# Optimization experiments

Hardware: AMD Instinct MI355X
Metric: run time of the kernel (lower is better)

Reference implementation:

```python
import jax, jax.numpy as jnp
import numpy as np
from jax import lax
from jax.scipy.special import logsumexp

V, E, H, S, L = 100000, 300, 256, 4096, 32   # vocab, word-emb, lstm hidden, seq len, max word len
NC, CE, CO = 64, 25, 25                      # char vocab, char emb dim, char-cnn out channels
T, START, STOP = 12, 10, 11                  # tagset


def setup_inputs() -> dict:
    key = jax.random.key(0)
    ks = jax.random.split(key, 20)
    s = 0.1
    inp = {
        "sentence": jax.random.randint(ks[0], (S,), 0, V),
        "chars": jax.random.randint(ks[1], (S, L), 0, NC),
        "tags": jax.random.randint(ks[2], (S,), 0, 9),
        "caps": jax.random.randint(ks[3], (S,), 0, 4),
        "word_embed": jax.random.normal(ks[4], (V, E), jnp.float32) * s,
        "char_embed": jax.random.normal(ks[5], (NC, CE), jnp.float32) * s,
        "conv_w": jax.random.normal(ks[6], (CO, 1, 3, CE), jnp.float32) * s,  # OIHW
        "conv_b": jnp.zeros((CO,), jnp.float32),
        "Wih_f": jax.random.normal(ks[7], (4 * H, E + CO), jnp.float32) * s,
        "Whh_f": jax.random.normal(ks[8], (4 * H, H), jnp.float32) * s,
        "b_f": jnp.zeros((4 * H,), jnp.float32),
        "Wih_b": jax.random.normal(ks[9], (4 * H, E + CO), jnp.float32) * s,
        "Whh_b": jax.random.normal(ks[10], (4 * H, H), jnp.float32) * s,
        "b_b": jnp.zeros((4 * H,), jnp.float32),
        "W_tag": jax.random.normal(ks[11], (T, 2 * H), jnp.float32) * s,
        "b_tag": jnp.zeros((T,), jnp.float32),
    }
    trans = jax.random.normal(ks[12], (T, T), jnp.float32)
    trans = trans.at[:, START].set(-10000.0).at[STOP, :].set(-10000.0)
    inp["transitions"] = trans
    return inp


def _lstm(xs, Wih, Whh, b):
    Hh = Whh.shape[1]

    def step(carry, x):
        h, c = carry
        g = x @ Wih.T + h @ Whh.T + b          # [4H]
        i, f, gg, o = jnp.split(g, 4)
        i, f, o = jax.nn.sigmoid(i), jax.nn.sigmoid(f), jax.nn.sigmoid(o)
        c = f * c + i * jnp.tanh(gg)
        h = o * jnp.tanh(c)
        return (h, c), h

    init = (jnp.zeros((Hh,), xs.dtype), jnp.zeros((Hh,), xs.dtype))
    _, hs = lax.scan(step, init, xs)
    return hs                                   # [S, H]


def reference(sentence, chars, tags, caps, word_embed, char_embed, conv_w, conv_b,
              Wih_f, Whh_f, b_f, Wih_b, Whh_b, b_b, W_tag, b_tag, transitions):
    # --- char CNN features ---
    ce = char_embed[chars][:, None, :, :]                      # [S,1,L,CE] (NCHW)
    conv = lax.conv_general_dilated(ce, conv_w, (1, 1), ((2, 2), (0, 0)),
                                    dimension_numbers=("NCHW", "OIHW", "NCHW"))
    conv = conv + conv_b[None, :, None, None]                  # [S,CO,L+2,1]
    char_feat = conv.max(axis=(2, 3))                          # [S,CO] (max-pool over time)

    # --- word + char embeddings (dropout = identity at eval) ---
    embeds = jnp.concatenate([word_embed[sentence], char_feat], axis=1)  # [S, E+CO]

    # --- BiLSTM ---
    hs_f = _lstm(embeds, Wih_f, Whh_f, b_f)
    hs_b = _lstm(embeds[::-1], Wih_b, Whh_b, b_b)[::-1]
    lstm_out = jnp.concatenate([hs_f, hs_b], axis=1)           # [S, 2H]
    feats = lstm_out @ W_tag.T + b_tag                         # [S, T]

    # --- CRF forward algorithm (log-sum-exp recurrence) ---
    alpha0 = jnp.full((T,), -10000.0, feats.dtype).at[START].set(0.0)

    def crf_step(alpha, feat):
        # smat[i,j] = alpha[i] + feat[j] + transitions[i,j]
        alpha = logsumexp(alpha[:, None] + feat[None, :] + transitions, axis=0)
        return alpha, None

    alpha, _ = lax.scan(crf_step, alpha0, feats)
    forward_score = logsumexp(alpha + transitions[:, STOP])

    # --- gold path score ---
    pad_start = jnp.concatenate([jnp.array([START]), tags])
    pad_stop = jnp.concatenate([tags, jnp.array([STOP])])
    gold = transitions[pad_start, pad_stop].sum() + feats[jnp.arange(S), tags].sum()

    return forward_score - gold                                # neg log likelihood (scalar)
```

## Files before the change

### kernel.cpp

```cpp
#include <hip/hip_runtime.h>
#include <cstdint>


#define S_LEN 4096
#define EMB_LD 328

typedef _Float16 half2_t __attribute__((ext_vector_type(2)));

__device__ __forceinline__ float fdot2(unsigned int a, unsigned int b, float acc) {
#if __has_builtin(__builtin_amdgcn_fdot2)
    return __builtin_amdgcn_fdot2(__builtin_bit_cast(half2_t, a),
                                  __builtin_bit_cast(half2_t, b), acc, false);
#else
    half2_t x = __builtin_bit_cast(half2_t, a);
    half2_t y = __builtin_bit_cast(half2_t, b);
    return acc + (float)x[0]*(float)y[0] + (float)x[1]*(float)y[1];
#endif
}

__device__ __forceinline__ unsigned int pack2f16(float a, float b) {
    union { _Float16 h[2]; unsigned int u; } v;
    v.h[0] = (_Float16)a; v.h[1] = (_Float16)b; return v.u;
}

__device__ __forceinline__ float sigm(float x) { return 1.0f / (1.0f + __expf(-x)); }

__device__ __forceinline__ float ftanh(float x) {
    float ax = fabsf(x);
    float e = __expf(-2.0f * ax);
    float t = (1.0f - e) / (1.0f + e);
    return copysignf(t, x);
}

static constexpr size_t WS_EMBEDS = 0;
static constexpr size_t WS_GI     = WS_EMBEDS + (size_t)4096*328*4;
static constexpr size_t WS_WP     = WS_GI     + (size_t)2*4096*1024*4;
static constexpr size_t WS_WL     = WS_WP     + (size_t)2*128*1024*4;
static constexpr size_t WS_CFEAT  = WS_WL     + (size_t)2*6*1024*16;
static constexpr size_t WS_HS     = WS_CFEAT  + (size_t)4096*25*4;
static constexpr size_t WS_FEATS  = WS_HS     + (size_t)2*4096*256*4;
static constexpr size_t WS_CHUNKS = WS_FEATS  + (size_t)4096*12*4;
static constexpr size_t WS_LVL2   = WS_CHUNKS + (size_t)256*144*4;
static constexpr size_t WS_SCAL   = WS_LVL2   + (size_t)16*144*4;

__global__ void k_pack(const float* __restrict__ whhf, const float* __restrict__ whhb,
                       unsigned int* __restrict__ wp, uint4* __restrict__ wl) {
    int idx = blockIdx.x * 256 + threadIdx.x;
    if (idx >= 2048) return;
    int dir = idx >> 10, row = idx & 1023;
    const float* W = (dir ? whhb : whhf) + row * 256;
    unsigned int* wpb = wp + (size_t)dir * 131072;
    #pragma unroll 4
    for (int kp = 0; kp < 104; kp++)
        wpb[kp * 1024 + row] = pack2f16(W[2*kp], W[2*kp + 1]);
    uint4* wlp = wl + (size_t)dir * 6 * 1024;
    for (int q = 0; q < 6; q++) {
        int e0 = 208 + 8 * q;
        uint4 v;
        v.x = pack2f16(W[e0+0], W[e0+1]);
        v.y = pack2f16(W[e0+2], W[e0+3]);
        v.z = pack2f16(W[e0+4], W[e0+5]);
        v.w = pack2f16(W[e0+6], W[e0+7]);
        wlp[q * 1024 + row] = v;
    }
}

__global__ void k_charcnn(const int* __restrict__ chars, const float* __restrict__ cemb,
                          const float* __restrict__ convw, const float* __restrict__ convb,
                          float* __restrict__ cfeat) {
    int s = blockIdx.x, tid = threadIdx.x;
    __shared__ float ce[32][25];
    __shared__ float wz[1875];
    __shared__ float bias[25];
    __shared__ float conv[850];
    for (int i = tid; i < 800; i += 128)
        ce[i / 25][i % 25] = cemb[chars[s * 32 + i / 25] * 25 + (i % 25)];
    for (int i = tid; i < 1875; i += 128) wz[i] = convw[i];
    if (tid < 25) bias[tid] = convb[tid];
    __syncthreads();
    for (int p = tid; p < 850; p += 128) {
        int tt = p / 25, o = p % 25;
        float acc = 0.f;
        #pragma unroll
        for (int kh = 0; kh < 3; kh++) {
            int tr = tt - 2 + kh;
            if (tr >= 0 && tr < 32) {
                const float* wrow = &wz[o * 75 + kh * 25];
                #pragma unroll
                for (int kw = 0; kw < 25; kw++) acc += ce[tr][kw] * wrow[kw];
            }
        }
        conv[p] = acc;
    }
    __syncthreads();
    if (tid < 25) {
        float m = conv[tid];
        for (int tt = 1; tt < 34; tt++) m = fmaxf(m, conv[tt * 25 + tid]);
        cfeat[s * 25 + tid] = m + bias[tid];
    }
}

__global__ void k_embeds(const int* __restrict__ sentence, const float* __restrict__ wemb,
                         const float* __restrict__ cfeat, float* __restrict__ embeds) {
    int s = blockIdx.x, tid = threadIdx.x;
    const float4* src = (const float4*)(wemb + (size_t)sentence[s] * 300);
    float4* dst = (float4*)(embeds + (size_t)s * EMB_LD);
    for (int i = tid; i < 75; i += 128) dst[i] = src[i];
    if (tid < 25) embeds[(size_t)s * EMB_LD + 300 + tid] = cfeat[s * 25 + tid];
    if (tid >= 25 && tid < 28) embeds[(size_t)s * EMB_LD + 325 + (tid - 25)] = 0.f;
}

__global__ __launch_bounds__(256) void k_gemm(const float* __restrict__ A,
        const float* __restrict__ Bf, const float* __restrict__ Bb,
        const float* __restrict__ bf, const float* __restrict__ bb,
        float* __restrict__ gi) {
    int bs = blockIdx.x;
    int br = blockIdx.y;
    int dir = br >> 4;
    int row0 = (br & 15) * 64;
    const float* B = dir ? Bb : Bf;
    const float* bias = dir ? bb : bf;
    __shared__ float As[16][65], Bs[16][65];
    int tid = threadIdx.x;
    int tx = tid & 15, ty = tid >> 4;
    int s0 = bs * 64;
    float acc[4][4] = {};
    int lr = tid >> 2, lc0 = (tid & 3) * 4;
    for (int k0 = 0; k0 < 325; k0 += 16) {
        #pragma unroll
        for (int i = 0; i < 4; i++) {
            int k = k0 + lc0 + i;
            As[lc0 + i][lr] = (k < 325) ? A[(size_t)(s0 + lr) * EMB_LD + k] : 0.f;
            Bs[lc0 + i][lr] = (k < 325) ? B[(size_t)(row0 + lr) * 325 + k] : 0.f;
        }
        __syncthreads();
        #pragma unroll
        for (int kk = 0; kk < 16; kk++) {
            float a[4], b[4];
            #pragma unroll
            for (int i = 0; i < 4; i++) a[i] = As[kk][ty * 4 + i];
            #pragma unroll
            for (int j = 0; j < 4; j++) b[j] = Bs[kk][tx * 4 + j];
            #pragma unroll
            for (int i = 0; i < 4; i++)
                #pragma unroll
                for (int j = 0; j < 4; j++) acc[i][j] += a[i] * b[j];
        }
        __syncthreads();
    }
    #pragma unroll
    for (int i = 0; i < 4; i++)
        #pragma unroll
        for (int j = 0; j < 4; j++) {
            int row = row0 + tx * 4 + j;
            int s   = s0 + ty * 4 + i;
            gi[(size_t)dir * 4194304 + (size_t)s * 1024 + row] = acc[i][j] + bias[row];
        }
}

#define LSTM_LDS_BYTES (98304 + 1024 + 2048)

__global__ __launch_bounds__(512, 2)
void k_lstm(const unsigned int* __restrict__ wp, const uint4* __restrict__ wl,
            const float* __restrict__ gi, float* __restrict__ hs) {
    const int dir = blockIdx.x;
    const int tid = threadIdx.x;
    extern __shared__ char smem[];
    uint4* tl          = (uint4*)smem;
    unsigned int* hbuf = (unsigned int*)(smem + 98304);
    float* gates       = (float*)(smem + 99328);

    unsigned int wra[104], wrb[104];
    const unsigned int* wpb = wp + (size_t)dir * 131072;
    #pragma unroll
    for (int kp = 0; kp < 104; kp++) {
        wra[kp] = wpb[kp * 1024 + tid];
        wrb[kp] = wpb[kp * 1024 + 512 + tid];
    }

    {
        const uint4* wlb = wl + (size_t)dir * (6 * 1024);
        for (int i = tid; i < 6144; i += 512) tl[i] = wlb[i];
    }
    if (tid < 256) hbuf[tid] = 0u;
    __syncthreads();

    const float* gib = gi + (size_t)dir * 4194304;
    const bool fw = (dir == 0);
    const int sq0 = fw ? 0 : (S_LEN - 1);
    const ptrdiff_t off = fw ? 1024 : -1024;
    const float* gptr = gib + (size_t)sq0 * 1024 + tid;
    float gpa = gptr[0];
    float gpb = gptr[512];

    float c = 0.f;
    const ptrdiff_t hoff = fw ? 256 : -256;
    float* hptr = hs + (size_t)dir * 1048576 + (size_t)sq0 * 256 + tid;

    #pragma clang loop unroll(disable)
    for (int s = 0; s < S_LEN; s++) {
        float gna = gptr[off];
        float gnb = gptr[off + 512];

        const uint4* hq = (const uint4*)(hbuf + (s & 1) * 128);
        float a0 = gpa, a1 = 0.f;
        float b0 = gpb, b1 = 0.f;
        #pragma unroll
        for (int m = 0; m < 26; m++) {
            uint4 h4 = hq[m];
            a0 = fdot2(wra[4*m+0], h4.x, a0);
            a1 = fdot2(wra[4*m+1], h4.y, a1);
            a0 = fdot2(wra[4*m+2], h4.z, a0);
            a1 = fdot2(wra[4*m+3], h4.w, a1);
            b0 = fdot2(wrb[4*m+0], h4.x, b0);
            b1 = fdot2(wrb[4*m+1], h4.y, b1);
            b0 = fdot2(wrb[4*m+2], h4.z, b0);
            b1 = fdot2(wrb[4*m+3], h4.w, b1);
        }
        #pragma unroll
        for (int q = 0; q < 6; q++) {
            uint4 ta = tl[q * 1024 + tid];
            uint4 tb = tl[q * 1024 + 512 + tid];
            uint4 h4 = hq[26 + q];
            a0 = fdot2(ta.x, h4.x, a0);
            a1 = fdot2(ta.y, h4.y, a1);
            a0 = fdot2(ta.z, h4.z, a0);
            a1 = fdot2(ta.w, h4.w, a1);
            b0 = fdot2(tb.x, h4.x, b0);
            b1 = fdot2(tb.y, h4.y, b1);
            b0 = fdot2(tb.z, h4.z, b0);
            b1 = fdot2(tb.w, h4.w, b1);
        }
        float va = a0 + a1;
        float vb = b0 + b1;
        if (tid >= 256) { gates[tid - 256] = va; gates[tid] = vb; }
        __syncthreads();

        if (tid < 256) {
            float ig = sigm(va);
            float fg = sigm(gates[tid]);
            float gt = ftanh(vb);
            float og = sigm(gates[256 + tid]);
            c = fg * c + ig * gt;
            float h = og * ftanh(c);
            *hptr = h; hptr += hoff;
            union { _Float16 hh; unsigned short u; } cv; cv.hh = (_Float16)h;
            ((unsigned short*)(hbuf + ((s + 1) & 1) * 128))[tid] = cv.u;
        }
        __syncthreads();
        gpa = gna; gpb = gnb;
        gptr += off;
    }
}

__global__ void k_feats(const float* __restrict__ hs, const float* __restrict__ wtag,
                        const float* __restrict__ btag, float* __restrict__ feats) {
    int s = blockIdx.x, j = threadIdx.x;
    if (j < 12) {
        const float* hf = hs + (size_t)s * 256;
        const float* hb = hs + 1048576 + (size_t)s * 256;
        const float* w = wtag + j * 512;
        float a0 = 0.f, a1 = 0.f, a2 = 0.f, a3 = 0.f;
        for (int k = 0; k < 256; k += 4) {
            a0 += hf[k] * w[k];     a1 += hf[k+1] * w[k+1];
            a2 += hf[k+2] * w[k+2]; a3 += hf[k+3] * w[k+3];
        }
        for (int k = 0; k < 256; k += 4) {
            a0 += hb[k] * w[256+k];     a1 += hb[k+1] * w[256+k+1];
            a2 += hb[k+2] * w[256+k+2]; a3 += hb[k+3] * w[256+k+3];
        }
        feats[s * 12 + j] = btag[j] + ((a0 + a1) + (a2 + a3));
    }
}

__global__ void k_gold(const float* __restrict__ feats, const int* __restrict__ tags,
                       const float* __restrict__ trans, float* __restrict__ scal) {
    __shared__ float red[256];
    int tid = threadIdx.x;
    float p = 0.f;
    for (int s = tid; s < S_LEN; s += 256) {
        int tg = tags[s];
        p += feats[s * 12 + tg];
        int prev = (s == 0) ? 10 : tags[s - 1];
        p += trans[prev * 12 + tg];
    }
    if (tid == 0) p += trans[tags[S_LEN - 1] * 12 + 11];
    red[tid] = p;
    __syncthreads();
    for (int off = 128; off; off >>= 1) {
        if (tid < off) red[tid] += red[tid + off];
        __syncthreads();
    }
    if (tid == 0) scal[0] = red[0];
}

__device__ __forceinline__ void lse_merge(const float* A, const float* B, float* C, int tid) {
    if (tid < 144) {
        int i = tid / 12, j = tid % 12;
        float m = -1e30f;
        #pragma unroll
        for (int k = 0; k < 12; k++) m = fmaxf(m, A[i * 12 + k] + B[k * 12 + j]);
        float sum = 0.f;
        #pragma unroll
        for (int k = 0; k < 12; k++) sum += __expf(A[i * 12 + k] + B[k * 12 + j] - m);
        C[tid] = m + __logf(sum);
    }
}

__global__ void k_crf1(const float* __restrict__ feats, const float* __restrict__ trans,
                       float* __restrict__ chunks) {
    int b = blockIdx.x, tid = threadIdx.x;
    __shared__ float A[144], Bv[144], Tr[144];
    if (tid < 144) Tr[tid] = trans[tid];
    int s0 = b * 16;
    if (tid < 144) A[tid] = trans[tid] + feats[s0 * 12 + (tid % 12)];
    __syncthreads();
    float* cur = A; float* nxt = Bv;
    for (int s = s0 + 1; s < s0 + 16; s++) {
        if (tid < 144) {
            int i = tid / 12, j = tid % 12;
            float m = -1e30f;
            #pragma unroll
            for (int k = 0; k < 12; k++) m = fmaxf(m, cur[i * 12 + k] + Tr[k * 12 + j]);
            float sum = 0.f;
            #pragma unroll
            for (int k = 0; k < 12; k++) sum += __expf(cur[i * 12 + k] + Tr[k * 12 + j] - m);
            nxt[tid] = feats[s * 12 + j] + m + __logf(sum);
        }
        __syncthreads();
        float* tmp = cur; cur = nxt; nxt = tmp;
    }
    if (tid < 144) chunks[b * 144 + tid] = cur[tid];
}

__global__ void k_crf2(const float* __restrict__ chunks, float* __restrict__ lvl2) {
    int b = blockIdx.x, tid = threadIdx.x;
    __shared__ float A[144], Bv[144], Cc[144];
    if (tid < 144) A[tid] = chunks[(size_t)(b * 16) * 144 + tid];
    __syncthreads();
    for (int m2 = 1; m2 < 16; m2++) {
        if (tid < 144) Bv[tid] = chunks[(size_t)(b * 16 + m2) * 144 + tid];
        __syncthreads();
        lse_merge(A, Bv, Cc, tid);
        __syncthreads();
        if (tid < 144) A[tid] = Cc[tid];
        __syncthreads();
    }
    if (tid < 144) lvl2[b * 144 + tid] = A[tid];
}

__global__ void k_crf3(const float* __restrict__ lvl2, const float* __restrict__ trans,
                       const float* __restrict__ scal, float* __restrict__ out) {
    __shared__ float A[144], Bv[144], Cc[144], alpha[12];
    int tid = threadIdx.x;
    if (tid < 144) A[tid] = lvl2[tid];
    __syncthreads();
    for (int m2 = 1; m2 < 16; m2++) {
        if (tid < 144) Bv[tid] = lvl2[m2 * 144 + tid];
        __syncthreads();
        lse_merge(A, Bv, Cc, tid);
        __syncthreads();
        if (tid < 144) A[tid] = Cc[tid];
        __syncthreads();
    }
    if (tid < 12) {
        int j = tid;
        float m = -1e30f;
        #pragma unroll
        for (int i = 0; i < 12; i++) {
            float v = ((i == 10) ? 0.f : -10000.f) + A[i * 12 + j];
            m = fmaxf(m, v);
        }
        float sum = 0.f;
        #pragma unroll
        for (int i = 0; i < 12; i++) {
            float v = ((i == 10) ? 0.f : -10000.f) + A[i * 12 + j];
            sum += __expf(v - m);
        }
        alpha[j] = m + __logf(sum) + trans[j * 12 + 11];
    }
    __syncthreads();
    if (tid == 0) {
        float m = -1e30f;
        #pragma unroll
        for (int j = 0; j < 12; j++) m = fmaxf(m, alpha[j]);
        float sum = 0.f;
        #pragma unroll
        for (int j = 0; j < 12; j++) sum += __expf(alpha[j] - m);
        out[0] = (m + __logf(sum)) - scal[0];
    }
}

extern "C" void kernel_launch(void* const* d_in, const int* in_sizes, int n_in,
                              void* d_out, int out_size, void* d_ws, size_t ws_size,
                              hipStream_t stream) {
    const int*   sentence = (const int*)d_in[0];
    const int*   chars    = (const int*)d_in[1];
    const int*   tags     = (const int*)d_in[2];
    const float* wemb     = (const float*)d_in[4];
    const float* cemb     = (const float*)d_in[5];
    const float* convw    = (const float*)d_in[6];
    const float* convb    = (const float*)d_in[7];
    const float* wihf     = (const float*)d_in[8];
    const float* whhf     = (const float*)d_in[9];
    const float* bf       = (const float*)d_in[10];
    const float* wihb     = (const float*)d_in[11];
    const float* whhb     = (const float*)d_in[12];
    const float* bb       = (const float*)d_in[13];
    const float* wtag     = (const float*)d_in[14];
    const float* btag     = (const float*)d_in[15];
    const float* trans    = (const float*)d_in[16];

    char* ws = (char*)d_ws;
    float*        embeds = (float*)(ws + WS_EMBEDS);
    float*        gi     = (float*)(ws + WS_GI);
    unsigned int* wp     = (unsigned int*)(ws + WS_WP);
    uint4*        wl     = (uint4*)(ws + WS_WL);
    float*        cfeat  = (float*)(ws + WS_CFEAT);
    float*        hsbuf  = (float*)(ws + WS_HS);
    float*        feats  = (float*)(ws + WS_FEATS);
    float*        chunks = (float*)(ws + WS_CHUNKS);
    float*        lvl2   = (float*)(ws + WS_LVL2);
    float*        scal   = (float*)(ws + WS_SCAL);

    hipFuncSetAttribute((const void*)k_lstm,
                        hipFuncAttributeMaxDynamicSharedMemorySize, LSTM_LDS_BYTES);

    k_pack<<<8, 256, 0, stream>>>(whhf, whhb, wp, wl);
    k_charcnn<<<4096, 128, 0, stream>>>(chars, cemb, convw, convb, cfeat);
    k_embeds<<<4096, 128, 0, stream>>>(sentence, wemb, cfeat, embeds);
    k_gemm<<<dim3(64, 32), 256, 0, stream>>>(embeds, wihf, wihb, bf, bb, gi);
    k_lstm<<<2, 512, LSTM_LDS_BYTES, stream>>>(wp, wl, gi, hsbuf);
    k_feats<<<4096, 64, 0, stream>>>(hsbuf, wtag, btag, feats);
    k_gold<<<1, 256, 0, stream>>>(feats, tags, trans, scal);
    k_crf1<<<256, 192, 0, stream>>>(feats, trans, chunks);
    k_crf2<<<16, 192, 0, stream>>>(chunks, lvl2);
    k_crf3<<<1, 192, 0, stream>>>(lvl2, trans, scal, (float*)d_out);
}
```

Before: 6.543 ms.

## Pair gate rows per lane and exchange via shuffle to drop one barrier

Reassigns LSTM gate rows so that adjacent lanes hold complementary gates (i/g and f/o) for the same cell. The lanes swap partial gate values with a cross-lane shuffle, which removes the LDS gates buffer and one __syncthreads per timestep. Both lanes now redundantly compute the cell update. The global store of h is deferred to the next iteration to take it off the critical path. The weight load pattern changes to strided rows, which may affect the initial load coalescing and LDS bank behavior for the tail weights.

```diff
diff --git a/kernel.cpp b/kernel.cpp
--- a/kernel.cpp
+++ b/kernel.cpp
@@ -158,24 +158,30 @@
         }
 }
 
-#define LSTM_LDS_BYTES (98304 + 1024 + 2048)
+#define LSTM_LDS_BYTES (98304 + 1024)
 
 __global__ __launch_bounds__(512, 2)
 void k_lstm(const unsigned int* __restrict__ wp, const uint4* __restrict__ wl,
             const float* __restrict__ gi, float* __restrict__ hs) {
-    const int dir = blockIdx.x;
-    const int tid = threadIdx.x;
+    const int dir  = blockIdx.x;
+    const int tid  = threadIdx.x;
+    const int w    = tid >> 6;
+    const int lane = tid & 63;
+    const int cell = w * 32 + (lane >> 1);
+    const int role = lane & 1;
+    const int rowA = role ? 256 + cell : cell;
+    const int rowB = role ? 768 + cell : 512 + cell;
+
     extern __shared__ char smem[];
     uint4* tl          = (uint4*)smem;
     unsigned int* hbuf = (unsigned int*)(smem + 98304);
-    float* gates       = (float*)(smem + 99328);
 
     unsigned int wra[104], wrb[104];
     const unsigned int* wpb = wp + (size_t)dir * 131072;
     #pragma unroll
     for (int kp = 0; kp < 104; kp++) {
-        wra[kp] = wpb[kp * 1024 + tid];
-        wrb[kp] = wpb[kp * 1024 + 512 + tid];
+        wra[kp] = wpb[kp * 1024 + rowA];
+        wrb[kp] = wpb[kp * 1024 + rowB];
     }
 
     {
@@ -189,18 +195,22 @@
     const bool fw = (dir == 0);
     const int sq0 = fw ? 0 : (S_LEN - 1);
     const ptrdiff_t off = fw ? 1024 : -1024;
-    const float* gptr = gib + (size_t)sq0 * 1024 + tid;
-    float gpa = gptr[0];
-    float gpb = gptr[512];
+    const float* gptrA = gib + (size_t)sq0 * 1024 + rowA;
+    const float* gptrB = gib + (size_t)sq0 * 1024 + rowB;
+    float gpa = *gptrA, gpb = *gptrB;
 
     float c = 0.f;
+    float hprev = 0.f;
     const ptrdiff_t hoff = fw ? 256 : -256;
-    float* hptr = hs + (size_t)dir * 1048576 + (size_t)sq0 * 256 + tid;
+    float* hptr = hs + (size_t)dir * 1048576 + (size_t)sq0 * 256 + cell;
 
     #pragma clang loop unroll(disable)
     for (int s = 0; s < S_LEN; s++) {
-        float gna = gptr[off];
-        float gnb = gptr[off + 512];
+        float gna = gptrA[off];
+        float gnb = gptrB[off];
+        gptrA += off; gptrB += off;
+
+        if (s > 0 && role == 0) { *hptr = hprev; hptr += hoff; }
 
         const uint4* hq = (const uint4*)(hbuf + (s & 1) * 128);
         float a0 = gpa, a1 = 0.f;
@@ -219,8 +229,8 @@
         }
         #pragma unroll
         for (int q = 0; q < 6; q++) {
-            uint4 ta = tl[q * 1024 + tid];
-            uint4 tb = tl[q * 1024 + 512 + tid];
+            uint4 ta = tl[q * 1024 + rowA];
+            uint4 tb = tl[q * 1024 + rowB];
             uint4 h4 = hq[26 + q];
             a0 = fdot2(ta.x, h4.x, a0);
             a1 = fdot2(ta.y, h4.y, a1);
@@ -233,24 +243,25 @@
         }
         float va = a0 + a1;
         float vb = b0 + b1;
-        if (tid >= 256) { gates[tid - 256] = va; gates[tid] = vb; }
-        __syncthreads();
-
-        if (tid < 256) {
-            float ig = sigm(va);
-            float fg = sigm(gates[tid]);
-            float gt = ftanh(vb);
-            float og = sigm(gates[256 + tid]);
-            c = fg * c + ig * gt;
-            float h = og * ftanh(c);
-            *hptr = h; hptr += hoff;
+
+        float pa = __shfl_xor(va, 1, 64);
+        float pb = __shfl_xor(vb, 1, 64);
+
+        float ig = sigm(va);
+        float fg = sigm(pa);
+        float gt = ftanh(vb);
+        float og = sigm(pb);
+        c = fg * c + ig * gt;
+        float h = og * ftanh(c);
+        hprev = h;
+        if (role == 0) {
             union { _Float16 hh; unsigned short u; } cv; cv.hh = (_Float16)h;
-            ((unsigned short*)(hbuf + ((s + 1) & 1) * 128))[tid] = cv.u;
+            ((unsigned short*)(hbuf + ((s + 1) & 1) * 128))[cell] = cv.u;
         }
         __syncthreads();
         gpa = gna; gpb = gnb;
-        gptr += off;
-    }
+    }
+    if (role == 0) *hptr = hprev;
 }
 
 __global__ void k_feats(const float* __restrict__ hs, const float* __restrict__ wtag,
```

After: 7.965 ms. 1.22x slower.

## Run LSTM recurrence with 1024 threads, one gate row each, exchanging gates via DPP

Applied to the files above, without the earlier changes.

The recurrent LSTM kernel now uses 1024 threads per direction, each owning a single gate row instead of two. Gate rows are interleaved so the four gates of a cell sit in adjacent lanes and are swapped with DPP quad permutes, which removes the shared-memory gate exchange and one barrier per step. The hidden-state buffer is triple-buffered so a single barrier per step is enough, and the gi layout and weight packing are permuted to match. Fewer weights stay in registers (92 pairs) and more are read from LDS each step (9 uint4), which trades register pressure for extra LDS traffic.

```diff
diff --git a/kernel.cpp b/kernel.cpp
--- a/kernel.cpp
+++ b/kernel.cpp
@@ -32,11 +32,24 @@
     return copysignf(t, x);
 }
 
+__device__ __forceinline__ float qxor1(float v) {
+    return __builtin_bit_cast(float, __builtin_amdgcn_mov_dpp(
+        __builtin_bit_cast(int, v), 0xB1, 0xF, 0xF, true));
+}
+__device__ __forceinline__ float qxor2(float v) {
+    return __builtin_bit_cast(float, __builtin_amdgcn_mov_dpp(
+        __builtin_bit_cast(int, v), 0x4E, 0xF, 0xF, true));
+}
+__device__ __forceinline__ float qxor3(float v) {
+    return __builtin_bit_cast(float, __builtin_amdgcn_mov_dpp(
+        __builtin_bit_cast(int, v), 0x1B, 0xF, 0xF, true));
+}
+
 static constexpr size_t WS_EMBEDS = 0;
 static constexpr size_t WS_GI     = WS_EMBEDS + (size_t)4096*328*4;
 static constexpr size_t WS_WP     = WS_GI     + (size_t)2*4096*1024*4;
-static constexpr size_t WS_WL     = WS_WP     + (size_t)2*128*1024*4;
-static constexpr size_t WS_CFEAT  = WS_WL     + (size_t)2*6*1024*16;
+static constexpr size_t WS_WL     = WS_WP     + (size_t)2*92*1024*4;
+static constexpr size_t WS_CFEAT  = WS_WL     + (size_t)2*9*1024*16;
 static constexpr size_t WS_HS     = WS_CFEAT  + (size_t)4096*25*4;
 static constexpr size_t WS_FEATS  = WS_HS     + (size_t)2*4096*256*4;
 static constexpr size_t WS_CHUNKS = WS_FEATS  + (size_t)4096*12*4;
@@ -49,19 +62,20 @@
     if (idx >= 2048) return;
     int dir = idx >> 10, row = idx & 1023;
     const float* W = (dir ? whhb : whhf) + row * 256;
-    unsigned int* wpb = wp + (size_t)dir * 131072;
+    int p = (row & 255) * 4 + (row >> 8);
+    unsigned int* wpb = wp + (size_t)dir * 92 * 1024;
     #pragma unroll 4
-    for (int kp = 0; kp < 104; kp++)
-        wpb[kp * 1024 + row] = pack2f16(W[2*kp], W[2*kp + 1]);
-    uint4* wlp = wl + (size_t)dir * 6 * 1024;
-    for (int q = 0; q < 6; q++) {
-        int e0 = 208 + 8 * q;
+    for (int kp = 0; kp < 92; kp++)
+        wpb[kp * 1024 + p] = pack2f16(W[2*kp], W[2*kp + 1]);
+    uint4* wlp = wl + (size_t)dir * 9 * 1024;
+    for (int q = 0; q < 9; q++) {
+        int e0 = 184 + 8 * q;
         uint4 v;
         v.x = pack2f16(W[e0+0], W[e0+1]);
         v.y = pack2f16(W[e0+2], W[e0+3]);
         v.z = pack2f16(W[e0+4], W[e0+5]);
         v.w = pack2f16(W[e0+6], W[e0+7]);
-        wlp[q * 1024 + row] = v;
+        wlp[q * 1024 + p] = v;
     }
 }
 
@@ -154,103 +168,93 @@
         for (int j = 0; j < 4; j++) {
             int row = row0 + tx * 4 + j;
             int s   = s0 + ty * 4 + i;
-            gi[(size_t)dir * 4194304 + (size_t)s * 1024 + row] = acc[i][j] + bias[row];
-        }
-}
-
-#define LSTM_LDS_BYTES (98304 + 1024 + 2048)
-
-__global__ __launch_bounds__(512, 2)
+            gi[(size_t)dir * 4194304 + (size_t)s * 1024 + (row & 255) * 4 + (row >> 8)]
+                = acc[i][j] + bias[row];
+        }
+}
+
+#define LSTM_LDS_BYTES (147456 + 1536)
+
+__global__ __launch_bounds__(1024, 4)
 void k_lstm(const unsigned int* __restrict__ wp, const uint4* __restrict__ wl,
             const float* __restrict__ gi, float* __restrict__ hs) {
-    const int dir = blockIdx.x;
-    const int tid = threadIdx.x;
+    const int dir  = blockIdx.x;
+    const int tid  = threadIdx.x;
+    const int cell = tid >> 2;
+    const int role = tid & 3;
+
     extern __shared__ char smem[];
     uint4* tl          = (uint4*)smem;
-    unsigned int* hbuf = (unsigned int*)(smem + 98304);
-    float* gates       = (float*)(smem + 99328);
-
-    unsigned int wra[104], wrb[104];
-    const unsigned int* wpb = wp + (size_t)dir * 131072;
+    unsigned int* hbuf = (unsigned int*)(smem + 147456);
+
+    unsigned int wr[92];
+    const unsigned int* wpb = wp + (size_t)dir * (92 * 1024);
     #pragma unroll
-    for (int kp = 0; kp < 104; kp++) {
-        wra[kp] = wpb[kp * 1024 + tid];
-        wrb[kp] = wpb[kp * 1024 + 512 + tid];
-    }
+    for (int kp = 0; kp < 92; kp++) wr[kp] = wpb[kp * 1024 + tid];
 
     {
-        const uint4* wlb = wl + (size_t)dir * (6 * 1024);
-        for (int i = tid; i < 6144; i += 512) tl[i] = wlb[i];
-    }
-    if (tid < 256) hbuf[tid] = 0u;
+        const uint4* wlb = wl + (size_t)dir * (9 * 1024);
+        for (int i = tid; i < 9216; i += 1024) tl[i] = wlb[i];
+    }
+    if (tid < 384) hbuf[tid] = 0u;
     __syncthreads();
 
     const float* gib = gi + (size_t)dir * 4194304;
+    float* hsb = hs + (size_t)dir * 1048576;
     const bool fw = (dir == 0);
     const int sq0 = fw ? 0 : (S_LEN - 1);
-    const ptrdiff_t off = fw ? 1024 : -1024;
-    const float* gptr = gib + (size_t)sq0 * 1024 + tid;
-    float gpa = gptr[0];
-    float gpb = gptr[512];
-
-    float c = 0.f;
-    const ptrdiff_t hoff = fw ? 256 : -256;
-    float* hptr = hs + (size_t)dir * 1048576 + (size_t)sq0 * 256 + tid;
+    float cst = 0.f, hprev = 0.f;
+    int sqprev = 0;
+    float gpre = gib[(size_t)sq0 * 1024 + tid];
 
     #pragma clang loop unroll(disable)
     for (int s = 0; s < S_LEN; s++) {
-        float gna = gptr[off];
-        float gnb = gptr[off + 512];
-
-        const uint4* hq = (const uint4*)(hbuf + (s & 1) * 128);
-        float a0 = gpa, a1 = 0.f;
-        float b0 = gpb, b1 = 0.f;
-        #pragma unroll
-        for (int m = 0; m < 26; m++) {
+        const int sq  = fw ? s : (S_LEN - 1 - s);
+        const int sn  = (s < S_LEN - 1) ? s + 1 : s;
+        const int sqn = fw ? sn : (S_LEN - 1 - sn);
+
+        if (s > 0 && role == 0) hsb[(size_t)sqprev * 256 + cell] = hprev;
+        float gnext = gib[(size_t)sqn * 1024 + tid];
+
+        const uint4* hq = (const uint4*)(hbuf + (s % 3) * 128);
+        float a0 = gpre, a1 = 0.f;
+        #pragma unroll
+        for (int m = 0; m < 23; m++) {
             uint4 h4 = hq[m];
-            a0 = fdot2(wra[4*m+0], h4.x, a0);
-            a1 = fdot2(wra[4*m+1], h4.y, a1);
-            a0 = fdot2(wra[4*m+2], h4.z, a0);
-            a1 = fdot2(wra[4*m+3], h4.w, a1);
-            b0 = fdot2(wrb[4*m+0], h4.x, b0);
-            b1 = fdot2(wrb[4*m+1], h4.y, b1);
-            b0 = fdot2(wrb[4*m+2], h4.z, b0);
-            b1 = fdot2(wrb[4*m+3], h4.w, b1);
-        }
-        #pragma unroll
-        for (int q = 0; q < 6; q++) {
-            uint4 ta = tl[q * 1024 + tid];
-            uint4 tb = tl[q * 1024 + 512 + tid];
-            uint4 h4 = hq[26 + q];
-            a0 = fdot2(ta.x, h4.x, a0);
-            a1 = fdot2(ta.y, h4.y, a1);
-            a0 = fdot2(ta.z, h4.z, a0);
-            a1 = fdot2(ta.w, h4.w, a1);
-            b0 = fdot2(tb.x, h4.x, b0);
-            b1 = fdot2(tb.y, h4.y, b1);
-            b0 = fdot2(tb.z, h4.z, b0);
-            b1 = fdot2(tb.w, h4.w, b1);
-        }
-        float va = a0 + a1;
-        float vb = b0 + b1;
-        if (tid >= 256) { gates[tid - 256] = va; gates[tid] = vb; }
-        __syncthreads();
-
-        if (tid < 256) {
-            float ig = sigm(va);
-            float fg = sigm(gates[tid]);
-            float gt = ftanh(vb);
-            float og = sigm(gates[256 + tid]);
-            c = fg * c + ig * gt;
-            float h = og * ftanh(c);
-            *hptr = h; hptr += hoff;
+            a0 = fdot2(wr[4*m+0], h4.x, a0);
+            a1 = fdot2(wr[4*m+1], h4.y, a1);
+            a0 = fdot2(wr[4*m+2], h4.z, a0);
+            a1 = fdot2(wr[4*m+3], h4.w, a1);
+        }
+        #pragma unroll
+        for (int q = 0; q < 9; q++) {
+            uint4 tw = tl[q * 1024 + tid];
+            uint4 h4 = hq[23 + q];
+            a0 = fdot2(tw.x, h4.x, a0);
+            a1 = fdot2(tw.y, h4.y, a1);
+            a0 = fdot2(tw.z, h4.z, a0);
+            a1 = fdot2(tw.w, h4.w, a1);
+        }
+        float val = a0 + a1;
+
+        float x1 = qxor1(val), x2 = qxor2(val), x3 = qxor3(val);
+        float vi = (role == 0) ? val : (role == 1) ? x1 : (role == 2) ? x2 : x3;
+        float vf = (role == 1) ? val : (role == 0) ? x1 : (role == 3) ? x2 : x3;
+        float vg = (role == 2) ? val : (role == 3) ? x1 : (role == 0) ? x2 : x3;
+        float vo = (role == 3) ? val : (role == 2) ? x1 : (role == 1) ? x2 : x3;
+
+        float ig = sigm(vi), fg = sigm(vf), gt = ftanh(vg), og = sigm(vo);
+        cst = fg * cst + ig * gt;
+        float h = og * ftanh(cst);
+        hprev = h; sqprev = sq;
+        if (role == 0) {
             union { _Float16 hh; unsigned short u; } cv; cv.hh = (_Float16)h;
-            ((unsigned short*)(hbuf + ((s + 1) & 1) * 128))[tid] = cv.u;
-        }
-        __syncthreads();
-        gpa = gna; gpb = gnb;
-        gptr += off;
-    }
+            ((unsigned short*)(hbuf + ((s + 1) % 3) * 128))[cell] = cv.u;
+        }
+        __syncthreads();
+        gpre = gnext;
+    }
+    if (role == 0) hsb[(size_t)sqprev * 256 + cell] = hprev;
 }
 
 __global__ void k_feats(const float* __restrict__ hs, const float* __restrict__ wtag,
@@ -430,7 +434,7 @@
     k_charcnn<<<4096, 128, 0, stream>>>(chars, cemb, convw, convb, cfeat);
     k_embeds<<<4096, 128, 0, stream>>>(sentence, wemb, cfeat, embeds);
     k_gemm<<<dim3(64, 32), 256, 0, stream>>>(embeds, wihf, wihb, bf, bb, gi);
-    k_lstm<<<2, 512, LSTM_LDS_BYTES, stream>>>(wp, wl, gi, hsbuf);
+    k_lstm<<<2, 1024, LSTM_LDS_BYTES, stream>>>(wp, wl, gi, hsbuf);
     k_feats<<<4096, 64, 0, stream>>>(hsbuf, wtag, btag, feats);
     k_gold<<<1, 256, 0, stream>>>(feats, tags, trans, scal);
     k_crf1<<<256, 192, 0, stream>>>(feats, trans, chunks);
```

Result: slower. 9.315 ms (+42.4%).
